# Kernel tuning notes

Hardware: AMD Instinct MI355X
Metric: run time of the kernel (lower is better)

The kernel has to match this reference:

```python
import jax, jax.numpy as jnp
import numpy as np

N_BLOCKS = 96
N = N_BLOCKS ** 2          # number of image blocks = n_blocks^2
D = 1024                   # feature dim (fixed by Linear(1024+1, 128))
EPS_COS = 1e-6             # eps of F.cosine_similarity
EPS_BN = 1e-5              # BatchNorm1d eps


def setup_inputs() -> dict:
    key = jax.random.key(0)
    ks = jax.random.split(key, 6)
    return {
        "features": jax.random.normal(ks[0], (N, D), dtype=jnp.float32),
        "scores": jax.random.uniform(ks[1], (N,), dtype=jnp.float32),
        "W1": jax.random.normal(ks[2], (D + 1, 128), dtype=jnp.float32) * 0.03,
        "b1": jnp.zeros((128,), jnp.float32),
        "g1": jnp.ones((128,), jnp.float32),
        "be1": jnp.zeros((128,), jnp.float32),
        "W2": jax.random.normal(ks[3], (128, 64), dtype=jnp.float32) * 0.08,
        "b2": jnp.zeros((64,), jnp.float32),
        "g2": jnp.ones((64,), jnp.float32),
        "be2": jnp.zeros((64,), jnp.float32),
        "W3": jax.random.normal(ks[4], (64, 1), dtype=jnp.float32) * 0.12,
        "b3": jnp.zeros((1,), jnp.float32),
    }


def _gaussian_similarity(features):
    # Vectorized form of the O(N^2) pairwise loop:
    #   cos_ij = <f_i, f_j> / max(|f_i||f_j|, eps)
    #   sigma^2 = D * (0.5 + 0.5 * cos)  ->  2*sigma^2 = D * (1 + cos)
    #   sim_ij = exp(-|f_i - f_j|^2 / (2*sigma^2)),  sim_ii = 1
    sq = jnp.sum(features * features, axis=-1)          # [N] squared norms
    gram = features @ features.T                          # [N, N] big GEMM
    norms = jnp.sqrt(sq)
    cos = gram / jnp.maximum(norms[:, None] * norms[None, :], EPS_COS)
    d2 = jnp.maximum(sq[:, None] + sq[None, :] - 2.0 * gram, 0.0)
    denom = jnp.maximum(jnp.float32(D) * (1.0 + cos), EPS_COS)
    sim = jnp.exp(-d2 / denom)
    eye = jnp.eye(sim.shape[0], dtype=bool)
    return jnp.where(eye, jnp.float32(1.0), sim)


def _bn_eval(h, gamma, beta):
    # BatchNorm1d in eval mode with init running stats (mean=0, var=1).
    return gamma * (h / jnp.sqrt(1.0 + EPS_BN)) + beta


def reference(features, scores, W1, b1, g1, be1, W2, b2, g2, be2, W3, b3):
    sim = _gaussian_similarity(features)                  # [N, N]
    x = jnp.concatenate([features, scores[:, None]], axis=1)  # [N, D+1]
    h = jax.nn.relu(_bn_eval(x @ W1 + b1, g1, be1))       # [N, 128]
    h = jax.nn.relu(_bn_eval(h @ W2 + b2, g2, be2))       # [N, 64]
    agg = jax.nn.sigmoid(h @ W3 + b3)[:, 0]               # [N]
    sim_mean = jnp.mean(sim, axis=1)                      # [N]
    # Torch broadcast [N,1] * [N] -> [N,N], then .mean() == mean(agg)*mean(sim_mean)
    return jnp.mean(agg) * jnp.mean(sim_mean)


if __name__ == "__main__":
    out = reference(**setup_inputs())
    print(out)
```

## Files before the change

### kernel.cpp

```cpp
#include <hip/hip_runtime.h>

#define N_IMG 9216
#define DFEAT 1024
#define NBC 36
#define NBR 72
#define NPAIR 1332

typedef __attribute__((ext_vector_type(8))) short short8;
typedef __attribute__((ext_vector_type(4))) float floatx4;
typedef __attribute__((ext_vector_type(16))) float floatx16;
typedef __attribute__((ext_vector_type(4))) int intx4;
typedef __attribute__((ext_vector_type(8))) int intx8;

__device__ __forceinline__ void async_copy16(const void* g, void* l) {
  __builtin_amdgcn_global_load_lds((const __attribute__((address_space(1))) void*)g,
                                   (__attribute__((address_space(3))) void*)l,
                                   16, 0, 0);
}

__device__ __forceinline__ unsigned short f2bf(float x) {
  union { float f; unsigned u; } a; a.f = x;
  unsigned u = a.u;
  u += 0x7fffu + ((u >> 16) & 1u);
  return (unsigned short)(u >> 16);
}

__device__ __forceinline__ size_t sw_decode(int P) {
  int L = P >> 3, ix = (P & 7) ^ (L & 7);
  return (size_t)(L * 2 + (ix >> 2)) * DFEAT + (size_t)(ix & 3) * 16;
}

__device__ __forceinline__ intx4 ld16s(const unsigned char* base, int r, int c) {
  int L = r >> 1, ix = (((r & 1) << 2) | c) ^ (L & 7);
  return *(const intx4*)(base + L * 128 + ix * 16);
}

__device__ __forceinline__ intx8 ldfrags(const unsigned char* base, int r, int kh) {
  intx4 lo = ld16s(base, r, kh * 2);
  intx4 hi = ld16s(base, r, kh * 2 + 1);
  intx8 v;
  v[0] = lo[0]; v[1] = lo[1]; v[2] = lo[2]; v[3] = lo[3];
  v[4] = hi[0]; v[5] = hi[1]; v[6] = hi[2]; v[7] = hi[3];
  return v;
}

__global__ __launch_bounds__(256) void convert_prep(const float* __restrict__ f,
                                                    const float* __restrict__ W1,
                                                    unsigned char* __restrict__ fb8,
                                                    float* __restrict__ sq,
                                                    float* __restrict__ rn,
                                                    unsigned short* __restrict__ W1t,
                                                    double* __restrict__ sums) {
  int b = blockIdx.x, t = threadIdx.x;
  if (b < 2304) {
    int lane = t & 63, wave = t >> 6;
    int row = b * 4 + wave;
    const float4* src = (const float4*)f + (size_t)row * 256;
    unsigned int* dst = (unsigned int*)(fb8 + (size_t)row * DFEAT);
    float s = 0.f;
#pragma unroll
    for (int j = 0; j < 4; j++) {
      float4 v = src[j * 64 + lane];
      s += v.x * v.x + v.y * v.y + v.z * v.z + v.w * v.w;
      int pk = __builtin_amdgcn_cvt_pk_fp8_f32(v.x, v.y, 0, false);
      pk = __builtin_amdgcn_cvt_pk_fp8_f32(v.z, v.w, pk, true);
      dst[j * 64 + lane] = (unsigned int)pk;
    }
#pragma unroll
    for (int off = 32; off > 0; off >>= 1) s += __shfl_down(s, off, 64);
    if (lane == 0) { sq[row] = s; rn[row] = rsqrtf(s); }
  } else {
    int j = b - 2304;
    if (j == 0 && t < 2) sums[t] = 0.0;
    for (int k = t; k < DFEAT; k += 256)
      W1t[(size_t)j * DFEAT + k] = f2bf(W1[(size_t)k * 128 + j]);
  }
}

__global__ __launch_bounds__(256, 2) void gram_sim(const unsigned char* __restrict__ fb8,
                                                   const float* __restrict__ sq,
                                                   const float* __restrict__ rn,
                                                   double* __restrict__ sums) {
  int rem = blockIdx.x, bcol = 0;
  for (;;) {
    int m = 2 * bcol + 2; if (m > NBR) m = NBR;
    if (rem < m) break;
    rem -= m; bcol++;
  }
  int brow = rem;

  __shared__ __align__(16) unsigned char Ab[2][8192];
  __shared__ __align__(16) unsigned char Bb[2][16384];
  __shared__ float sqA[128], rnA[128], sqB[256], rnB[256];
  __shared__ float wpart[4];

  int t = threadIdx.x, lane = t & 63, wave = t >> 6;
  if (t < 128) { sqA[t] = sq[brow * 128 + t]; rnA[t] = rn[brow * 128 + t]; }
  sqB[t] = sq[bcol * 256 + t];
  rnB[t] = rn[bcol * 256 + t];

  const unsigned char* Asrc = fb8 + (size_t)brow * 128 * DFEAT;
  const unsigned char* Bsrc = fb8 + (size_t)bcol * 256 * DFEAT;

  const size_t d0 = sw_decode(t);
  const size_t d1 = sw_decode(t + 256);
  const size_t d2 = sw_decode(t + 512);
  const size_t d3 = sw_decode(t + 768);

  floatx16 acc[2][4];
#pragma unroll
  for (int mi = 0; mi < 2; mi++)
#pragma unroll
    for (int ni = 0; ni < 4; ni++)
#pragma unroll
      for (int e = 0; e < 16; e++) acc[mi][ni][e] = 0.f;

  const int wr = (wave & 1) * 64, wc = (wave >> 1) * 128;
  const int r32 = lane & 31, kh = lane >> 5;

  async_copy16(Asrc + d0, &Ab[0][t * 16]);
  async_copy16(Asrc + d1, &Ab[0][(t + 256) * 16]);
  async_copy16(Bsrc + d0, &Bb[0][t * 16]);
  async_copy16(Bsrc + d1, &Bb[0][(t + 256) * 16]);
  async_copy16(Bsrc + d2, &Bb[0][(t + 512) * 16]);
  async_copy16(Bsrc + d3, &Bb[0][(t + 768) * 16]);

  for (int kb = 0; kb < 16; kb++) {
    __syncthreads();
    if (kb < 15) {
      const int nb = (kb + 1) & 1;
      const size_t k0 = (size_t)(kb + 1) * 64;
      async_copy16(Asrc + d0 + k0, &Ab[nb][t * 16]);
      async_copy16(Asrc + d1 + k0, &Ab[nb][(t + 256) * 16]);
      async_copy16(Bsrc + d0 + k0, &Bb[nb][t * 16]);
      async_copy16(Bsrc + d1 + k0, &Bb[nb][(t + 256) * 16]);
      async_copy16(Bsrc + d2 + k0, &Bb[nb][(t + 512) * 16]);
      async_copy16(Bsrc + d3 + k0, &Bb[nb][(t + 768) * 16]);
    }
    const unsigned char* Ac = Ab[kb & 1];
    const unsigned char* Bc = Bb[kb & 1];
    intx8 a[2], b[4];
#pragma unroll
    for (int mi = 0; mi < 2; mi++) a[mi] = ldfrags(Ac, wr + mi * 32 + r32, kh);
#pragma unroll
    for (int ni = 0; ni < 4; ni++) b[ni] = ldfrags(Bc, wc + ni * 32 + r32, kh);
#pragma unroll
    for (int mi = 0; mi < 2; mi++)
#pragma unroll
      for (int ni = 0; ni < 4; ni++)
        acc[mi][ni] = __builtin_amdgcn_mfma_scale_f32_32x32x64_f8f6f4(
            a[mi], b[ni], acc[mi][ni], 0, 0, 0, 0x7F7F7F7F, 0, 0x7F7F7F7F);
  }

  const bool interior = (brow < 2 * bcol);
  float lsum = 0.f;
#pragma unroll
  for (int ni = 0; ni < 4; ni++) {
    int j_loc = wc + ni * 32 + r32;
    float sj = sqB[j_loc], rnj = rnB[j_loc];
    int j_g = bcol * 256 + j_loc;
#pragma unroll
    for (int mi = 0; mi < 2; mi++) {
      int rbase = wr + mi * 32 + 4 * kh;
#pragma unroll
      for (int reg = 0; reg < 16; reg++) {
        int i_loc = rbase + (reg & 3) + 8 * (reg >> 2);
        float gv = acc[mi][ni][reg];
        float si = sqA[i_loc], rni = rnA[i_loc];
        float cosv = gv * rni * rnj;
        float den = fmaf(1024.f, cosv, 1024.f);
        float d2 = si + sj - (gv + gv);
        float sim = __builtin_amdgcn_exp2f(-d2 * __builtin_amdgcn_rcpf(den) * 1.44269504f);
        if (interior) {
          lsum += sim;
        } else {
          int i_g = brow * 128 + i_loc;
          lsum += (i_g < j_g) ? 2.f * sim : (i_g == j_g ? 1.f : 0.f);
        }
      }
    }
  }
  if (interior) lsum *= 2.f;
#pragma unroll
  for (int off = 32; off > 0; off >>= 1) lsum += __shfl_down(lsum, off, 64);
  if (lane == 0) wpart[wave] = lsum;
  __syncthreads();
  if (t == 0)
    atomicAdd(&sums[0], (double)(wpart[0] + wpart[1] + wpart[2] + wpart[3]));
}

__global__ __launch_bounds__(256) void mlp_full(const float* __restrict__ f,
                                                const unsigned short* __restrict__ W1t,
                                                const float* __restrict__ scores,
                                                const float* __restrict__ W1,
                                                const float* __restrict__ b1,
                                                const float* __restrict__ g1,
                                                const float* __restrict__ be1,
                                                const float* __restrict__ W2, const float* __restrict__ b2,
                                                const float* __restrict__ g2, const float* __restrict__ be2,
                                                const float* __restrict__ W3, const float* __restrict__ b3,
                                                double* __restrict__ sums) {
  int r0 = blockIdx.x * 64;

  __shared__ __align__(16) float As32[64 * 32];
  __shared__ __align__(16) unsigned short Bs[128 * 32];
  __shared__ float h1s[64][128];
  __shared__ float h2s[64][65];
  __shared__ float sc[64], b1s[128], g1s[128], be1s[128], wls[128], ls[64];

  int t = threadIdx.x, lane = t & 63, wave = t >> 6;
  if (t < 64) sc[t] = scores[r0 + t];
  if (t < 128) {
    b1s[t] = b1[t]; g1s[t] = g1[t]; be1s[t] = be1[t];
    wls[t] = W1[(size_t)DFEAT * 128 + t];
  }

  floatx4 acc[2][4];
#pragma unroll
  for (int a = 0; a < 2; a++)
#pragma unroll
    for (int b = 0; b < 4; b++) acc[a][b] = (floatx4){0.f, 0.f, 0.f, 0.f};

  const int wr = (wave & 1) * 32, wc = (wave >> 1) * 64;

  for (int k0 = 0; k0 < DFEAT; k0 += 32) {
    __syncthreads();
    {
      int c = t, rA = c >> 3, p = c & 7, l = p ^ (rA & 7);
      async_copy16(f + (size_t)(r0 + rA) * DFEAT + k0 + l * 4, (char*)As32 + c * 16);
      c = t + 256; rA = c >> 3; p = c & 7; l = p ^ (rA & 7);
      async_copy16(f + (size_t)(r0 + rA) * DFEAT + k0 + l * 4, (char*)As32 + c * 16);
      c = t; int rB = c >> 2; p = c & 3; l = p ^ (rB & 3);
      async_copy16(W1t + (size_t)rB * DFEAT + k0 + l * 8, (char*)Bs + c * 16);
      c = t + 256; rB = c >> 2; p = c & 3; l = p ^ (rB & 3);
      async_copy16(W1t + (size_t)rB * DFEAT + k0 + l * 8, (char*)Bs + c * 16);
    }
    __syncthreads();

    const int mrow = lane & 15, kq = (lane >> 4) * 8;
    short8 a[2], b[4];
#pragma unroll
    for (int mt = 0; mt < 2; mt++) {
      int row = wr + mt * 16 + mrow;
      int l0 = kq >> 2;
      int p0 = l0 ^ (row & 7), p1 = (l0 + 1) ^ (row & 7);
      float4 f0 = *(const float4*)&As32[row * 32 + p0 * 4];
      float4 f1 = *(const float4*)&As32[row * 32 + p1 * 4];
      short8 af;
      af[0] = (short)f2bf(f0.x); af[1] = (short)f2bf(f0.y);
      af[2] = (short)f2bf(f0.z); af[3] = (short)f2bf(f0.w);
      af[4] = (short)f2bf(f1.x); af[5] = (short)f2bf(f1.y);
      af[6] = (short)f2bf(f1.z); af[7] = (short)f2bf(f1.w);
      a[mt] = af;
    }
#pragma unroll
    for (int nt = 0; nt < 4; nt++) {
      int row = wc + nt * 16 + mrow;
      int p = (kq >> 3) ^ (row & 3);
      b[nt] = *(const short8*)&Bs[row * 32 + p * 8];
    }
#pragma unroll
    for (int mt = 0; mt < 2; mt++)
#pragma unroll
      for (int nt = 0; nt < 4; nt++)
        acc[mt][nt] = __builtin_amdgcn_mfma_f32_16x16x32_bf16(a[mt], b[nt], acc[mt][nt], 0, 0, 0);
  }

  const float inv = 1.0f / sqrtf(1.0f + 1e-5f);
  const int rq = (lane >> 4) * 4, cn = lane & 15;
#pragma unroll
  for (int nt = 0; nt < 4; nt++) {
    int j = wc + nt * 16 + cn;
    float bj = b1s[j], gj = g1s[j] * inv, bej = be1s[j], wj = wls[j];
#pragma unroll
    for (int mt = 0; mt < 2; mt++) {
#pragma unroll
      for (int rr = 0; rr < 4; rr++) {
        int iL = wr + mt * 16 + rq + rr;
        float pre = acc[mt][nt][rr] + sc[iL] * wj + bj;
        h1s[iL][j] = fmaxf(gj * pre + bej, 0.f);
      }
    }
  }
  __syncthreads();

  {
    int j = t & 63, rg = (t >> 6) * 16;
    float a2[16];
#pragma unroll
    for (int rr = 0; rr < 16; rr++) a2[rr] = 0.f;
    for (int k = 0; k < 128; k++) {
      float w = W2[k * 64 + j];
#pragma unroll
      for (int rr = 0; rr < 16; rr++) a2[rr] = fmaf(h1s[rg + rr][k], w, a2[rr]);
    }
    float scv = g2[j] * inv, bi = b2[j], be = be2[j];
#pragma unroll
    for (int rr = 0; rr < 16; rr++)
      h2s[rg + rr][j] = fmaxf(scv * (a2[rr] + bi) + be, 0.f);
  }
  __syncthreads();

  if (t < 64) {
    float z = b3[0];
#pragma unroll
    for (int k = 0; k < 64; k++) z = fmaf(h2s[t][k], W3[k], z);
    ls[t] = 1.f / (1.f + __expf(-z));
  }
  __syncthreads();
  if (t == 0) {
    float s = 0.f;
#pragma unroll
    for (int iL = 0; iL < 64; iL++) s += ls[iL];
    atomicAdd(&sums[1], (double)s);
  }
}

__global__ void finalize(const double* __restrict__ sums, float* __restrict__ out) {
  double simmean = sums[0] / ((double)N_IMG * (double)N_IMG);
  double aggmean = sums[1] / (double)N_IMG;
  out[0] = (float)(aggmean * simmean);
}

extern "C" void kernel_launch(void* const* d_in, const int* in_sizes, int n_in,
                              void* d_out, int out_size, void* d_ws, size_t ws_size,
                              hipStream_t stream) {
  const float* f      = (const float*)d_in[0];
  const float* scores = (const float*)d_in[1];
  const float* W1 = (const float*)d_in[2];
  const float* b1 = (const float*)d_in[3];
  const float* g1 = (const float*)d_in[4];
  const float* be1 = (const float*)d_in[5];
  const float* W2 = (const float*)d_in[6];
  const float* b2 = (const float*)d_in[7];
  const float* g2 = (const float*)d_in[8];
  const float* be2 = (const float*)d_in[9];
  const float* W3 = (const float*)d_in[10];
  const float* b3 = (const float*)d_in[11];

  char* ws = (char*)d_ws;
  unsigned char* fb8  = (unsigned char*)ws;
  float* sq           = (float*)(ws + 9437184);
  float* rn           = (float*)(ws + 9474048);
  unsigned short* W1t = (unsigned short*)(ws + 9510912);
  double* sums        = (double*)(ws + 9773056);

  convert_prep<<<2432, 256, 0, stream>>>(f, W1, fb8, sq, rn, W1t, sums);
  gram_sim<<<NPAIR, 256, 0, stream>>>(fb8, sq, rn, sums);
  mlp_full<<<144, 256, 0, stream>>>(f, W1t, scores, W1, b1, g1, be1,
                                    W2, b2, g2, be2, W3, b3, sums);
  finalize<<<1, 1, 0, stream>>>(sums, (float*)d_out);
}
```

Before: 204.5 us.

## Fuse MLP into gram kernel, pre-normalize fp8 features, simplify similarity epilogue

Merges the MLP kernel into the gram/similarity launch by giving the first 144 blocks the MLP role and overlaying their shared memory in a union, which removes one launch and lets the MLP overlap with the gram work. Features are normalized before fp8 conversion, so the MFMA result is the cosine directly. The epilogue is rewritten as a single exp2 of an FMA with precomputed per-row constants, replacing the separate d2 and denominator arithmetic. The LDS swizzle scheme also changes. Normalizing before quantization changes fp8 rounding behaviour, and the union may raise per-block LDS use for the gram path.

```diff
diff --git a/kernel.cpp b/kernel.cpp
--- a/kernel.cpp
+++ b/kernel.cpp
@@ -2,9 +2,9 @@
 
 #define N_IMG 9216
 #define DFEAT 1024
-#define NBC 36
 #define NBR 72
 #define NPAIR 1332
+#define NMLP 144
 
 typedef __attribute__((ext_vector_type(8))) short short8;
 typedef __attribute__((ext_vector_type(4))) float floatx4;
@@ -12,6 +12,9 @@
 typedef __attribute__((ext_vector_type(4))) int intx4;
 typedef __attribute__((ext_vector_type(8))) int intx8;
 
+#define C1F 0.0014088818759657845f
+#define C2F 0.05308355472172724f
+
 __device__ __forceinline__ void async_copy16(const void* g, void* l) {
   __builtin_amdgcn_global_load_lds((const __attribute__((address_space(1))) void*)g,
                                    (__attribute__((address_space(3))) void*)l,
@@ -25,16 +28,17 @@
   return (unsigned short)(u >> 16);
 }
 
-__device__ __forceinline__ size_t sw_decode(int P) {
-  int L = P >> 3, ix = (P & 7) ^ (L & 7);
-  return (size_t)(L * 2 + (ix >> 2)) * DFEAT + (size_t)(ix & 3) * 16;
-}
-
+__device__ __forceinline__ size_t sw_src(int P) {
+  int L = P >> 3, s = P & 7;
+  int row = 2 * L + (s & 1);
+  int c = ((s >> 1) - L) & 3;
+  return (size_t)row * DFEAT + (size_t)c * 16;
+}
 __device__ __forceinline__ intx4 ld16s(const unsigned char* base, int r, int c) {
-  int L = r >> 1, ix = (((r & 1) << 2) | c) ^ (L & 7);
-  return *(const intx4*)(base + L * 128 + ix * 16);
-}
-
+  int L = r >> 1;
+  int slot = (((c + L) & 3) << 1) | (r & 1);
+  return *(const intx4*)(base + L * 128 + slot * 16);
+}
 __device__ __forceinline__ intx8 ldfrags(const unsigned char* base, int r, int kh) {
   intx4 lo = ld16s(base, r, kh * 2);
   intx4 hi = ld16s(base, r, kh * 2 + 1);
@@ -47,8 +51,8 @@
 __global__ __launch_bounds__(256) void convert_prep(const float* __restrict__ f,
                                                     const float* __restrict__ W1,
                                                     unsigned char* __restrict__ fb8,
-                                                    float* __restrict__ sq,
-                                                    float* __restrict__ rn,
+                                                    float* __restrict__ sL,
+                                                    float* __restrict__ pL,
                                                     unsigned short* __restrict__ W1t,
                                                     double* __restrict__ sums) {
   int b = blockIdx.x, t = threadIdx.x;
@@ -57,18 +61,26 @@
     int row = b * 4 + wave;
     const float4* src = (const float4*)f + (size_t)row * 256;
     unsigned int* dst = (unsigned int*)(fb8 + (size_t)row * DFEAT);
-    float s = 0.f;
+    float4 v0 = src[lane], v1 = src[64 + lane], v2 = src[128 + lane], v3 = src[192 + lane];
+    float s = v0.x * v0.x + v0.y * v0.y + v0.z * v0.z + v0.w * v0.w
+            + v1.x * v1.x + v1.y * v1.y + v1.z * v1.z + v1.w * v1.w
+            + v2.x * v2.x + v2.y * v2.y + v2.z * v2.z + v2.w * v2.w
+            + v3.x * v3.x + v3.y * v3.y + v3.z * v3.z + v3.w * v3.w;
+#pragma unroll
+    for (int off = 32; off > 0; off >>= 1) s += __shfl_xor(s, off, 64);
+    float rinv = rsqrtf(s);
+    float4 vv[4] = {v0, v1, v2, v3};
 #pragma unroll
     for (int j = 0; j < 4; j++) {
-      float4 v = src[j * 64 + lane];
-      s += v.x * v.x + v.y * v.y + v.z * v.z + v.w * v.w;
-      int pk = __builtin_amdgcn_cvt_pk_fp8_f32(v.x, v.y, 0, false);
-      pk = __builtin_amdgcn_cvt_pk_fp8_f32(v.z, v.w, pk, true);
+      float4 v = vv[j];
+      int pk = __builtin_amdgcn_cvt_pk_fp8_f32(v.x * rinv, v.y * rinv, 0, false);
+      pk = __builtin_amdgcn_cvt_pk_fp8_f32(v.z * rinv, v.w * rinv, pk, true);
       dst[j * 64 + lane] = (unsigned int)pk;
     }
-#pragma unroll
-    for (int off = 32; off > 0; off >>= 1) s += __shfl_down(s, off, 64);
-    if (lane == 0) { sq[row] = s; rn[row] = rsqrtf(s); }
+    if (lane == 0) {
+      sL[row] = s * C1F;
+      pL[row] = sqrtf(s) * C2F;
+    }
   } else {
     int j = b - 2304;
     if (j == 0 && t < 2) sums[t] = 0.0;
@@ -77,142 +89,157 @@
   }
 }
 
-__global__ __launch_bounds__(256, 2) void gram_sim(const unsigned char* __restrict__ fb8,
-                                                   const float* __restrict__ sq,
-                                                   const float* __restrict__ rn,
-                                                   double* __restrict__ sums) {
-  int rem = blockIdx.x, bcol = 0;
-  for (;;) {
-    int m = 2 * bcol + 2; if (m > NBR) m = NBR;
-    if (rem < m) break;
-    rem -= m; bcol++;
-  }
-  int brow = rem;
-
-  __shared__ __align__(16) unsigned char Ab[2][8192];
-  __shared__ __align__(16) unsigned char Bb[2][16384];
-  __shared__ float sqA[128], rnA[128], sqB[256], rnB[256];
-  __shared__ float wpart[4];
+__global__ __launch_bounds__(256, 2) void gram_mlp(
+    const unsigned char* __restrict__ fb8,
+    const float* __restrict__ sL, const float* __restrict__ pL,
+    const float* __restrict__ f, const unsigned short* __restrict__ W1t,
+    const float* __restrict__ scores, const float* __restrict__ W1,
+    const float* __restrict__ b1, const float* __restrict__ g1,
+    const float* __restrict__ be1,
+    const float* __restrict__ W2, const float* __restrict__ b2,
+    const float* __restrict__ g2, const float* __restrict__ be2,
+    const float* __restrict__ W3, const float* __restrict__ b3,
+    double* __restrict__ sums) {
+  __shared__ union __align__(16) SMem {
+    struct {
+      unsigned char Ab[2][8192];
+      unsigned char Bb[2][16384];
+      float sA[128], pA[128], sB[256], pB[256];
+      float wpart[4];
+    } g;
+    struct {
+      float As32[64 * 32];
+      unsigned short Bs[128 * 32];
+      float h1s[64][128];
+      float h2s[64][65];
+      float sc[64], b1s[128], g1s[128], be1s[128], wls[128], ls[64];
+    } m;
+  } sm;
 
   int t = threadIdx.x, lane = t & 63, wave = t >> 6;
-  if (t < 128) { sqA[t] = sq[brow * 128 + t]; rnA[t] = rn[brow * 128 + t]; }
-  sqB[t] = sq[bcol * 256 + t];
-  rnB[t] = rn[bcol * 256 + t];
-
-  const unsigned char* Asrc = fb8 + (size_t)brow * 128 * DFEAT;
-  const unsigned char* Bsrc = fb8 + (size_t)bcol * 256 * DFEAT;
-
-  const size_t d0 = sw_decode(t);
-  const size_t d1 = sw_decode(t + 256);
-  const size_t d2 = sw_decode(t + 512);
-  const size_t d3 = sw_decode(t + 768);
-
-  floatx16 acc[2][4];
-#pragma unroll
-  for (int mi = 0; mi < 2; mi++)
-#pragma unroll
-    for (int ni = 0; ni < 4; ni++)
-#pragma unroll
-      for (int e = 0; e < 16; e++) acc[mi][ni][e] = 0.f;
-
-  const int wr = (wave & 1) * 64, wc = (wave >> 1) * 128;
-  const int r32 = lane & 31, kh = lane >> 5;
-
-  async_copy16(Asrc + d0, &Ab[0][t * 16]);
-  async_copy16(Asrc + d1, &Ab[0][(t + 256) * 16]);
-  async_copy16(Bsrc + d0, &Bb[0][t * 16]);
-  async_copy16(Bsrc + d1, &Bb[0][(t + 256) * 16]);
-  async_copy16(Bsrc + d2, &Bb[0][(t + 512) * 16]);
-  async_copy16(Bsrc + d3, &Bb[0][(t + 768) * 16]);
-
-  for (int kb = 0; kb < 16; kb++) {
-    __syncthreads();
-    if (kb < 15) {
-      const int nb = (kb + 1) & 1;
-      const size_t k0 = (size_t)(kb + 1) * 64;
-      async_copy16(Asrc + d0 + k0, &Ab[nb][t * 16]);
-      async_copy16(Asrc + d1 + k0, &Ab[nb][(t + 256) * 16]);
-      async_copy16(Bsrc + d0 + k0, &Bb[nb][t * 16]);
-      async_copy16(Bsrc + d1 + k0, &Bb[nb][(t + 256) * 16]);
-      async_copy16(Bsrc + d2 + k0, &Bb[nb][(t + 512) * 16]);
-      async_copy16(Bsrc + d3 + k0, &Bb[nb][(t + 768) * 16]);
-    }
-    const unsigned char* Ac = Ab[kb & 1];
-    const unsigned char* Bc = Bb[kb & 1];
-    intx8 a[2], b[4];
-#pragma unroll
-    for (int mi = 0; mi < 2; mi++) a[mi] = ldfrags(Ac, wr + mi * 32 + r32, kh);
-#pragma unroll
-    for (int ni = 0; ni < 4; ni++) b[ni] = ldfrags(Bc, wc + ni * 32 + r32, kh);
+
+  if (blockIdx.x >= NMLP) {
+    int rem = blockIdx.x - NMLP, bcol = 0;
+    for (;;) {
+      int mlim = 2 * bcol + 2; if (mlim > NBR) mlim = NBR;
+      if (rem < mlim) break;
+      rem -= mlim; bcol++;
+    }
+    int brow = rem;
+
+    if (t < 128) { sm.g.sA[t] = sL[brow * 128 + t]; sm.g.pA[t] = pL[brow * 128 + t]; }
+    sm.g.sB[t] = sL[bcol * 256 + t];
+    sm.g.pB[t] = pL[bcol * 256 + t];
+
+    const unsigned char* Asrc = fb8 + (size_t)brow * 128 * DFEAT;
+    const unsigned char* Bsrc = fb8 + (size_t)bcol * 256 * DFEAT;
+
+    const size_t d0 = sw_src(t);
+    const size_t d1 = sw_src(t + 256);
+    const size_t d2 = sw_src(t + 512);
+    const size_t d3 = sw_src(t + 768);
+
+    floatx16 acc[2][4];
 #pragma unroll
     for (int mi = 0; mi < 2; mi++)
 #pragma unroll
       for (int ni = 0; ni < 4; ni++)
-        acc[mi][ni] = __builtin_amdgcn_mfma_scale_f32_32x32x64_f8f6f4(
-            a[mi], b[ni], acc[mi][ni], 0, 0, 0, 0x7F7F7F7F, 0, 0x7F7F7F7F);
-  }
-
-  const bool interior = (brow < 2 * bcol);
-  float lsum = 0.f;
-#pragma unroll
-  for (int ni = 0; ni < 4; ni++) {
-    int j_loc = wc + ni * 32 + r32;
-    float sj = sqB[j_loc], rnj = rnB[j_loc];
-    int j_g = bcol * 256 + j_loc;
+#pragma unroll
+        for (int e = 0; e < 16; e++) acc[mi][ni][e] = 0.f;
+
+    const int wr = (wave & 1) * 64, wc = (wave >> 1) * 128;
+    const int r32 = lane & 31, kh = lane >> 5;
+
+    async_copy16(Asrc + d0, &sm.g.Ab[0][t * 16]);
+    async_copy16(Asrc + d1, &sm.g.Ab[0][(t + 256) * 16]);
+    async_copy16(Bsrc + d0, &sm.g.Bb[0][t * 16]);
+    async_copy16(Bsrc + d1, &sm.g.Bb[0][(t + 256) * 16]);
+    async_copy16(Bsrc + d2, &sm.g.Bb[0][(t + 512) * 16]);
+    async_copy16(Bsrc + d3, &sm.g.Bb[0][(t + 768) * 16]);
+
+    for (int kb = 0; kb < 16; kb++) {
+      __syncthreads();
+      if (kb < 15) {
+        const int nb = (kb + 1) & 1;
+        const size_t k0 = (size_t)(kb + 1) * 64;
+        async_copy16(Asrc + d0 + k0, &sm.g.Ab[nb][t * 16]);
+        async_copy16(Asrc + d1 + k0, &sm.g.Ab[nb][(t + 256) * 16]);
+        async_copy16(Bsrc + d0 + k0, &sm.g.Bb[nb][t * 16]);
+        async_copy16(Bsrc + d1 + k0, &sm.g.Bb[nb][(t + 256) * 16]);
+        async_copy16(Bsrc + d2 + k0, &sm.g.Bb[nb][(t + 512) * 16]);
+        async_copy16(Bsrc + d3 + k0, &sm.g.Bb[nb][(t + 768) * 16]);
+      }
+      const unsigned char* Ac = sm.g.Ab[kb & 1];
+      const unsigned char* Bc = sm.g.Bb[kb & 1];
+      intx8 a[2], b[4];
+#pragma unroll
+      for (int mi = 0; mi < 2; mi++) a[mi] = ldfrags(Ac, wr + mi * 32 + r32, kh);
+#pragma unroll
+      for (int ni = 0; ni < 4; ni++) b[ni] = ldfrags(Bc, wc + ni * 32 + r32, kh);
+#pragma unroll
+      for (int mi = 0; mi < 2; mi++)
+#pragma unroll
+        for (int ni = 0; ni < 4; ni++)
+          acc[mi][ni] = __builtin_amdgcn_mfma_scale_f32_32x32x64_f8f6f4(
+              a[mi], b[ni], acc[mi][ni], 0, 0, 0, 0x7F7F7F7F, 0, 0x7F7F7F7F);
+    }
+
+    const bool interior = (brow < 2 * bcol);
+    float lsum = 0.f;
 #pragma unroll
     for (int mi = 0; mi < 2; mi++) {
-      int rbase = wr + mi * 32 + 4 * kh;
+      const int rbase = wr + mi * 32 + 4 * kh;
+      float si[16], pi[16];
 #pragma unroll
       for (int reg = 0; reg < 16; reg++) {
         int i_loc = rbase + (reg & 3) + 8 * (reg >> 2);
-        float gv = acc[mi][ni][reg];
-        float si = sqA[i_loc], rni = rnA[i_loc];
-        float cosv = gv * rni * rnj;
-        float den = fmaf(1024.f, cosv, 1024.f);
-        float d2 = si + sj - (gv + gv);
-        float sim = __builtin_amdgcn_exp2f(-d2 * __builtin_amdgcn_rcpf(den) * 1.44269504f);
+        si[reg] = sm.g.sA[i_loc];
+        pi[reg] = sm.g.pA[i_loc];
+      }
+#pragma unroll
+      for (int ni = 0; ni < 4; ni++) {
+        int j_loc = wc + ni * 32 + r32;
+        float sj = sm.g.sB[j_loc], pj = sm.g.pB[j_loc];
         if (interior) {
-          lsum += sim;
+#pragma unroll
+          for (int reg = 0; reg < 16; reg++) {
+            float u = acc[mi][ni][reg];
+            float r = __builtin_amdgcn_rcpf(1.f + u);
+            float del = pi[reg] * pj;
+            float gam = si[reg] + sj + del;
+            lsum += __builtin_amdgcn_exp2f(fmaf(-gam, r, del));
+          }
         } else {
-          int i_g = brow * 128 + i_loc;
-          lsum += (i_g < j_g) ? 2.f * sim : (i_g == j_g ? 1.f : 0.f);
+          int j_g = bcol * 256 + j_loc;
+#pragma unroll
+          for (int reg = 0; reg < 16; reg++) {
+            int i_g = brow * 128 + rbase + (reg & 3) + 8 * (reg >> 2);
+            float u = acc[mi][ni][reg];
+            float r = __builtin_amdgcn_rcpf(1.f + u);
+            float del = pi[reg] * pj;
+            float gam = si[reg] + sj + del;
+            float sim = __builtin_amdgcn_exp2f(fmaf(-gam, r, del));
+            lsum += (i_g < j_g) ? 2.f * sim : (i_g == j_g ? 1.f : 0.f);
+          }
         }
       }
     }
-  }
-  if (interior) lsum *= 2.f;
-#pragma unroll
-  for (int off = 32; off > 0; off >>= 1) lsum += __shfl_down(lsum, off, 64);
-  if (lane == 0) wpart[wave] = lsum;
-  __syncthreads();
-  if (t == 0)
-    atomicAdd(&sums[0], (double)(wpart[0] + wpart[1] + wpart[2] + wpart[3]));
-}
-
-__global__ __launch_bounds__(256) void mlp_full(const float* __restrict__ f,
-                                                const unsigned short* __restrict__ W1t,
-                                                const float* __restrict__ scores,
-                                                const float* __restrict__ W1,
-                                                const float* __restrict__ b1,
-                                                const float* __restrict__ g1,
-                                                const float* __restrict__ be1,
-                                                const float* __restrict__ W2, const float* __restrict__ b2,
-                                                const float* __restrict__ g2, const float* __restrict__ be2,
-                                                const float* __restrict__ W3, const float* __restrict__ b3,
-                                                double* __restrict__ sums) {
+    if (interior) lsum *= 2.f;
+#pragma unroll
+    for (int off = 32; off > 0; off >>= 1) lsum += __shfl_down(lsum, off, 64);
+    if (lane == 0) sm.g.wpart[wave] = lsum;
+    __syncthreads();
+    if (t == 0)
+      atomicAdd(&sums[0],
+                (double)(sm.g.wpart[0] + sm.g.wpart[1] + sm.g.wpart[2] + sm.g.wpart[3]));
+    return;
+  }
+
   int r0 = blockIdx.x * 64;
-
-  __shared__ __align__(16) float As32[64 * 32];
-  __shared__ __align__(16) unsigned short Bs[128 * 32];
-  __shared__ float h1s[64][128];
-  __shared__ float h2s[64][65];
-  __shared__ float sc[64], b1s[128], g1s[128], be1s[128], wls[128], ls[64];
-
-  int t = threadIdx.x, lane = t & 63, wave = t >> 6;
-  if (t < 64) sc[t] = scores[r0 + t];
+  if (t < 64) sm.m.sc[t] = scores[r0 + t];
   if (t < 128) {
-    b1s[t] = b1[t]; g1s[t] = g1[t]; be1s[t] = be1[t];
-    wls[t] = W1[(size_t)DFEAT * 128 + t];
+    sm.m.b1s[t] = b1[t]; sm.m.g1s[t] = g1[t]; sm.m.be1s[t] = be1[t];
+    sm.m.wls[t] = W1[(size_t)DFEAT * 128 + t];
   }
 
   floatx4 acc[2][4];
@@ -227,13 +254,13 @@
     __syncthreads();
     {
       int c = t, rA = c >> 3, p = c & 7, l = p ^ (rA & 7);
-      async_copy16(f + (size_t)(r0 + rA) * DFEAT + k0 + l * 4, (char*)As32 + c * 16);
+      async_copy16(f + (size_t)(r0 + rA) * DFEAT + k0 + l * 4, (char*)sm.m.As32 + c * 16);
       c = t + 256; rA = c >> 3; p = c & 7; l = p ^ (rA & 7);
-      async_copy16(f + (size_t)(r0 + rA) * DFEAT + k0 + l * 4, (char*)As32 + c * 16);
+      async_copy16(f + (size_t)(r0 + rA) * DFEAT + k0 + l * 4, (char*)sm.m.As32 + c * 16);
       c = t; int rB = c >> 2; p = c & 3; l = p ^ (rB & 3);
-      async_copy16(W1t + (size_t)rB * DFEAT + k0 + l * 8, (char*)Bs + c * 16);
+      async_copy16(W1t + (size_t)rB * DFEAT + k0 + l * 8, (char*)sm.m.Bs + c * 16);
       c = t + 256; rB = c >> 2; p = c & 3; l = p ^ (rB & 3);
-      async_copy16(W1t + (size_t)rB * DFEAT + k0 + l * 8, (char*)Bs + c * 16);
+      async_copy16(W1t + (size_t)rB * DFEAT + k0 + l * 8, (char*)sm.m.Bs + c * 16);
     }
     __syncthreads();
 
@@ -244,8 +271,8 @@
       int row = wr + mt * 16 + mrow;
       int l0 = kq >> 2;
       int p0 = l0 ^ (row & 7), p1 = (l0 + 1) ^ (row & 7);
-      float4 f0 = *(const float4*)&As32[row * 32 + p0 * 4];
-      float4 f1 = *(const float4*)&As32[row * 32 + p1 * 4];
+      float4 f0 = *(const float4*)&sm.m.As32[row * 32 + p0 * 4];
+      float4 f1 = *(const float4*)&sm.m.As32[row * 32 + p1 * 4];
       short8 af;
       af[0] = (short)f2bf(f0.x); af[1] = (short)f2bf(f0.y);
       af[2] = (short)f2bf(f0.z); af[3] = (short)f2bf(f0.w);
@@ -257,7 +284,7 @@
     for (int nt = 0; nt < 4; nt++) {
       int row = wc + nt * 16 + mrow;
       int p = (kq >> 3) ^ (row & 3);
-      b[nt] = *(const short8*)&Bs[row * 32 + p * 8];
+      b[nt] = *(const short8*)&sm.m.Bs[row * 32 + p * 8];
     }
 #pragma unroll
     for (int mt = 0; mt < 2; mt++)
@@ -271,14 +298,14 @@
 #pragma unroll
   for (int nt = 0; nt < 4; nt++) {
     int j = wc + nt * 16 + cn;
-    float bj = b1s[j], gj = g1s[j] * inv, bej = be1s[j], wj = wls[j];
+    float bj = sm.m.b1s[j], gj = sm.m.g1s[j] * inv, bej = sm.m.be1s[j], wj = sm.m.wls[j];
 #pragma unroll
     for (int mt = 0; mt < 2; mt++) {
 #pragma unroll
       for (int rr = 0; rr < 4; rr++) {
         int iL = wr + mt * 16 + rq + rr;
-        float pre = acc[mt][nt][rr] + sc[iL] * wj + bj;
-        h1s[iL][j] = fmaxf(gj * pre + bej, 0.f);
+        float pre = acc[mt][nt][rr] + sm.m.sc[iL] * wj + bj;
+        sm.m.h1s[iL][j] = fmaxf(gj * pre + bej, 0.f);
       }
     }
   }
@@ -292,26 +319,26 @@
     for (int k = 0; k < 128; k++) {
       float w = W2[k * 64 + j];
 #pragma unroll
-      for (int rr = 0; rr < 16; rr++) a2[rr] = fmaf(h1s[rg + rr][k], w, a2[rr]);
+      for (int rr = 0; rr < 16; rr++) a2[rr] = fmaf(sm.m.h1s[rg + rr][k], w, a2[rr]);
     }
     float scv = g2[j] * inv, bi = b2[j], be = be2[j];
 #pragma unroll
     for (int rr = 0; rr < 16; rr++)
-      h2s[rg + rr][j] = fmaxf(scv * (a2[rr] + bi) + be, 0.f);
+      sm.m.h2s[rg + rr][j] = fmaxf(scv * (a2[rr] + bi) + be, 0.f);
   }
   __syncthreads();
 
   if (t < 64) {
     float z = b3[0];
 #pragma unroll
-    for (int k = 0; k < 64; k++) z = fmaf(h2s[t][k], W3[k], z);
-    ls[t] = 1.f / (1.f + __expf(-z));
+    for (int k = 0; k < 64; k++) z = fmaf(sm.m.h2s[t][k], W3[k], z);
+    sm.m.ls[t] = 1.f / (1.f + __expf(-z));
   }
   __syncthreads();
   if (t == 0) {
     float s = 0.f;
 #pragma unroll
-    for (int iL = 0; iL < 64; iL++) s += ls[iL];
+    for (int iL = 0; iL < 64; iL++) s += sm.m.ls[iL];
     atomicAdd(&sums[1], (double)s);
   }
 }
@@ -340,14 +367,13 @@
 
   char* ws = (char*)d_ws;
   unsigned char* fb8  = (unsigned char*)ws;
-  float* sq           = (float*)(ws + 9437184);
-  float* rn           = (float*)(ws + 9474048);
+  float* sL           = (float*)(ws + 9437184);
+  float* pL           = (float*)(ws + 9474048);
   unsigned short* W1t = (unsigned short*)(ws + 9510912);
   double* sums        = (double*)(ws + 9773056);
 
-  convert_prep<<<2432, 256, 0, stream>>>(f, W1, fb8, sq, rn, W1t, sums);
-  gram_sim<<<NPAIR, 256, 0, stream>>>(fb8, sq, rn, sums);
-  mlp_full<<<144, 256, 0, stream>>>(f, W1t, scores, W1, b1, g1, be1,
-                                    W2, b2, g2, be2, W3, b3, sums);
+  convert_prep<<<2432, 256, 0, stream>>>(f, W1, fb8, sL, pL, W1t, sums);
+  gram_mlp<<<NMLP + NPAIR, 256, 0, stream>>>(fb8, sL, pL, f, W1t, scores, W1,
+                                             b1, g1, be1, W2, b2, g2, be2, W3, b3, sums);
   finalize<<<1, 1, 0, stream>>>(sums, (float*)d_out);
 }
```

Result: slower. 450.7 us (+120.4%).
